# Kernel optimization log

Hardware: AMD Instinct MI355X
Metric: run time of the kernel (lower is better)

## Reference

```python
import jax, jax.numpy as jnp
import numpy as np

NUM_HEADS = 8

def setup_inputs() -> dict:
    key = jax.random.key(0)
    ks = jax.random.split(key, 10)
    B, S, D = 4, 2048, 512
    scale = 1.0 / np.sqrt(D)
    return {
        "x": jax.random.normal(ks[0], (B, S, D), dtype=jnp.float32),
        "q": jax.random.normal(ks[1], (B, S, D), dtype=jnp.float32),
        "Wq": jax.random.normal(ks[2], (D, D), dtype=jnp.float32) * scale,
        "bq": jax.random.normal(ks[3], (D,), dtype=jnp.float32) * 0.01,
        "Wk": jax.random.normal(ks[4], (D, D), dtype=jnp.float32) * scale,
        "bk": jax.random.normal(ks[5], (D,), dtype=jnp.float32) * 0.01,
        "Wv": jax.random.normal(ks[6], (D, D), dtype=jnp.float32) * scale,
        "bv": jax.random.normal(ks[7], (D,), dtype=jnp.float32) * 0.01,
        "Wo": jax.random.normal(ks[8], (D, D), dtype=jnp.float32) * scale,
        "bo": jax.random.normal(ks[9], (D,), dtype=jnp.float32) * 0.01,
    }

def reference(x, q, Wq, bq, Wk, bk, Wv, bv, Wo, bo):
    B, S, D = x.shape
    H = NUM_HEADS
    Dh = D // H
    # Linear layers: y = x @ W.T + b (torch nn.Linear convention)
    def split_heads(t):  # [B,S,D] -> [B,H,S,Dh]
        return t.reshape(B, -1, H, Dh).transpose(0, 2, 1, 3)
    Q = split_heads(q @ Wq.T + bq)
    K = split_heads(x @ Wk.T + bk)
    V = split_heads(x @ Wv.T + bv)
    logits = jnp.einsum('bhqd,bhkd->bhqk', Q, K) / jnp.sqrt(jnp.asarray(Dh, Q.dtype))
    attn = jax.nn.softmax(logits, axis=-1)
    out = jnp.einsum('bhqk,bhkd->bhqd', attn, V)  # [B,H,S,Dh]
    concat = out.transpose(0, 2, 1, 3).reshape(B, -1, D)
    return concat @ Wo.T + bo
```

## Files before the change

kernel.cpp:

```cpp
#include <hip/hip_runtime.h>
#include <stdint.h>

typedef __bf16 bf16_t;
typedef bf16_t bf16x8 __attribute__((ext_vector_type(8)));
typedef bf16_t bf16x4 __attribute__((ext_vector_type(4)));
typedef bf16_t bf16x2 __attribute__((ext_vector_type(2)));
typedef float f32x4 __attribute__((ext_vector_type(4)));
typedef float f32x16 __attribute__((ext_vector_type(16)));
typedef uint32_t u32x4 __attribute__((ext_vector_type(4)));

#define DEV __device__ __forceinline__

DEV void gload_lds16(const void* g, void* l) {
  __builtin_amdgcn_global_load_lds(
      (__attribute__((address_space(1))) void*)(g),
      (__attribute__((address_space(3))) void*)(l), 16, 0, 0);
}

__global__ __launch_bounds__(256) void cvt2_kernel(
    const float* __restrict__ x, const float* __restrict__ q,
    bf16_t* __restrict__ xb, bf16_t* __restrict__ qb) {
  const float* s = blockIdx.y ? q : x;
  bf16_t* d = blockIdx.y ? qb : xb;
  int i = blockIdx.x * 256 + threadIdx.x;
  if (i < 524288) {
    const float4* sp = (const float4*)s + (size_t)i * 2;
    float4 a = sp[0], b = sp[1];
    bf16x8 o;
    o[0] = (bf16_t)a.x; o[1] = (bf16_t)a.y; o[2] = (bf16_t)a.z; o[3] = (bf16_t)a.w;
    o[4] = (bf16_t)b.x; o[5] = (bf16_t)b.y; o[6] = (bf16_t)b.z; o[7] = (bf16_t)b.w;
    *(bf16x8*)(d + (size_t)i * 8) = o;
  }
}

__global__ __launch_bounds__(256) void cvtw_kernel(
    const float* __restrict__ Wq, const float* __restrict__ Wk,
    const float* __restrict__ Wv, const float* __restrict__ Wo,
    bf16_t* __restrict__ dst) {
  int y = blockIdx.y;
  const float* s = (y == 0) ? Wq : (y == 1) ? Wk : (y == 2) ? Wv : Wo;
  bf16_t* d = dst + (size_t)y * 262144;
  int i = blockIdx.x * 256 + threadIdx.x;
  if (i < 32768) {
    const float4* sp = (const float4*)s + (size_t)i * 2;
    float4 a = sp[0], b = sp[1];
    bf16x8 o;
    o[0] = (bf16_t)a.x; o[1] = (bf16_t)a.y; o[2] = (bf16_t)a.z; o[3] = (bf16_t)a.w;
    o[4] = (bf16_t)b.x; o[5] = (bf16_t)b.y; o[6] = (bf16_t)b.z; o[7] = (bf16_t)b.w;
    *(bf16x8*)(d + (size_t)i * 8) = o;
  }
}

DEV void gemm_core(const bf16_t* __restrict__ A, const bf16_t* __restrict__ W,
                   char* smem, f32x4 (&acc)[4][4]) {
  const int tid = threadIdx.x;
  const int lane = tid & 63;
  const int wid = tid >> 6;
  const int wr = wid >> 1, wc = wid & 1;
  const int bx = blockIdx.x, by = blockIdx.y;

  uint32_t goffA[4], goffB[4], ldsoff[4];
#pragma unroll
  for (int c = 0; c < 4; ++c) {
    uint32_t o = (uint32_t)wid * 4096u + (uint32_t)c * 1024u + (uint32_t)lane * 16u;
    uint32_t row = o >> 7;
    uint32_t inner = (o & 127u) ^ ((row & 7u) << 4);
    goffA[c] = ((uint32_t)by * 128u + row) * 1024u + inner;
    goffB[c] = ((uint32_t)bx * 128u + row) * 1024u + inner;
    ldsoff[c] = o - (uint32_t)lane * 16u;
  }
  uint32_t offA[4][2], offB[4][2];
#pragma unroll
  for (int i = 0; i < 4; ++i)
#pragma unroll
    for (int kk = 0; kk < 2; ++kk) {
      uint32_t ra = (uint32_t)(wr * 64 + i * 16 + (lane & 15));
      offA[i][kk] = ra * 128u + (((uint32_t)kk * 64u + ((lane >> 4) * 16u)) ^ ((ra & 7u) << 4));
      uint32_t rb = (uint32_t)(wc * 64 + i * 16 + (lane & 15));
      offB[i][kk] = rb * 128u + (((uint32_t)kk * 64u + ((lane >> 4) * 16u)) ^ ((rb & 7u) << 4));
    }

  const char* Ab = (const char*)A;
  const char* Wb = (const char*)W;

#pragma unroll
  for (int c = 0; c < 4; ++c) {
    gload_lds16(Ab + goffA[c], smem + ldsoff[c]);
    gload_lds16(Wb + goffB[c], smem + 16384 + ldsoff[c]);
  }
  asm volatile("s_waitcnt vmcnt(0)" ::: "memory");
  __syncthreads();

#pragma unroll 1
  for (int kt = 0; kt < 8; ++kt) {
    const int buf = kt & 1;
    char* cur = smem + buf * 32768;
    if (kt < 7) {
      char* nxt = smem + (buf ^ 1) * 32768;
      uint32_t gk = (uint32_t)(kt + 1) * 128u;
#pragma unroll
      for (int c = 0; c < 4; ++c) {
        gload_lds16(Ab + goffA[c] + gk, nxt + ldsoff[c]);
        gload_lds16(Wb + goffB[c] + gk, nxt + 16384 + ldsoff[c]);
      }
    }
    bf16x8 af[4][2], bfr[4][2];
#pragma unroll
    for (int kk = 0; kk < 2; ++kk)
#pragma unroll
      for (int i = 0; i < 4; ++i) {
        af[i][kk] = *(const bf16x8*)(cur + offA[i][kk]);
        bfr[i][kk] = *(const bf16x8*)(cur + 16384 + offB[i][kk]);
      }
    __builtin_amdgcn_s_setprio(1);
#pragma unroll
    for (int kk = 0; kk < 2; ++kk)
#pragma unroll
      for (int mi = 0; mi < 4; ++mi)
#pragma unroll
        for (int nj = 0; nj < 4; ++nj)
          acc[mi][nj] = __builtin_amdgcn_mfma_f32_16x16x32_bf16(
              af[mi][kk], bfr[nj][kk], acc[mi][nj], 0, 0, 0);
    __builtin_amdgcn_s_setprio(0);
    asm volatile("s_waitcnt vmcnt(0)" ::: "memory");
    __syncthreads();
  }
}

__global__ __launch_bounds__(256) void gemm_qkv_kernel(
    const bf16_t* __restrict__ xb, const bf16_t* __restrict__ qb,
    const bf16_t* __restrict__ Wb, const float* __restrict__ bq,
    const float* __restrict__ bk, const float* __restrict__ bv,
    bf16_t* __restrict__ Qh, bf16_t* __restrict__ Kh, bf16_t* __restrict__ VT) {
  __shared__ char smem[65536];
  const int z = blockIdx.z;
  const bf16_t* A = (z == 0) ? qb : xb;
  const bf16_t* W = Wb + (size_t)z * 262144;
  const float* bias = (z == 0) ? bq : (z == 1) ? bk : bv;

  f32x4 acc[4][4] = {};
  gemm_core(A, W, smem, acc);

  const int lane = threadIdx.x & 63, wid = threadIdx.x >> 6;
  const int wr = wid >> 1, wc = wid & 1;
  const int colbase = blockIdx.x * 128 + wc * 64 + (lane & 15);
  const int rowbase = blockIdx.y * 128 + wr * 64 + ((lane >> 4) << 2);

  if (z == 2) {
#pragma unroll
    for (int nj = 0; nj < 4; ++nj) {
      int c = colbase + nj * 16;
      float bb = bias[c];
      int h = c >> 6, d = c & 63;
#pragma unroll
      for (int mi = 0; mi < 4; ++mi) {
        int r0 = rowbase + mi * 16;
        int b = r0 >> 11, s0 = r0 & 2047;
        bf16x4 v;
#pragma unroll
        for (int rr = 0; rr < 4; ++rr) v[rr] = (bf16_t)(acc[mi][nj][rr] + bb);
        *(bf16x4*)(VT + ((size_t)((b << 3) | h) * 64 + d) * 2048 + s0) = v;
      }
    }
  } else {
    bf16_t* O = (z == 0) ? Qh : Kh;
    const float scl = (z == 0) ? 0.18033688f : 1.0f;
#pragma unroll
    for (int nj = 0; nj < 4; ++nj) {
      int c = colbase + nj * 16;
      float bb = bias[c];
      int h = c >> 6, d = c & 63;
#pragma unroll
      for (int mi = 0; mi < 4; ++mi)
#pragma unroll
        for (int rr = 0; rr < 4; ++rr) {
          int r = rowbase + mi * 16 + rr;
          int b = r >> 11, s = r & 2047;
          O[((size_t)((b << 3) | h) * 2048 + s) * 64 + d] = (bf16_t)((acc[mi][nj][rr] + bb) * scl);
        }
    }
  }
}

__global__ __launch_bounds__(256) void gemm_out_kernel(
    const bf16_t* __restrict__ ctx, const bf16_t* __restrict__ Wo,
    const float* __restrict__ bo, float* __restrict__ out) {
  __shared__ char smem[65536];
  f32x4 acc[4][4] = {};
  gemm_core(ctx, Wo, smem, acc);

  const int lane = threadIdx.x & 63, wid = threadIdx.x >> 6;
  const int wr = wid >> 1, wc = wid & 1;
  const int colbase = blockIdx.x * 128 + wc * 64 + (lane & 15);
  const int rowbase = blockIdx.y * 128 + wr * 64 + ((lane >> 4) << 2);
#pragma unroll
  for (int nj = 0; nj < 4; ++nj) {
    int c = colbase + nj * 16;
    float bb = bo[c];
#pragma unroll
    for (int mi = 0; mi < 4; ++mi)
#pragma unroll
      for (int rr = 0; rr < 4; ++rr) {
        int r = rowbase + mi * 16 + rr;
        out[(size_t)r * 512 + c] = acc[mi][nj][rr] + bb;
      }
  }
}

__global__ __launch_bounds__(256, 2) void attn_kernel(
    const bf16_t* __restrict__ Qh, const bf16_t* __restrict__ Kh,
    const bf16_t* __restrict__ VT, bf16_t* __restrict__ ctx) {
  __shared__ char smem[32768];
  char* Kb = smem;
  char* Vb = smem + 16384;
  const int tid = threadIdx.x, lane = tid & 63, wid = tid >> 6;
  const int l31 = lane & 31, h = lane >> 5;
  const int qt = blockIdx.x, bh = blockIdx.y;

  const char* Kbase = (const char*)Kh + (size_t)bh * 262144;
  const char* Vbase = (const char*)VT + (size_t)bh * 262144;
  const char* Qbase = (const char*)Qh + (size_t)bh * 262144;

  const int qrow = qt * 128 + wid * 32 + l31;
  bf16x8 qf[4];
#pragma unroll
  for (int ks = 0; ks < 4; ++ks)
    qf[ks] = *(const bf16x8*)(Qbase + (size_t)qrow * 128 + ks * 32 + h * 16);

  uint32_t kgo[2], vgo[2], lo[2];
#pragma unroll
  for (int c = 0; c < 2; ++c) {
    uint32_t o = (uint32_t)c * 4096u + (uint32_t)wid * 1024u + (uint32_t)lane * 16u;
    uint32_t row = o >> 7;
    uint32_t inner = (o & 127u) ^ ((row & 7u) << 4);
    kgo[c] = row * 128u + inner;
    vgo[c] = row * 4096u + inner;
    lo[c] = o - (uint32_t)lane * 16u;
  }

  const uint32_t swz = (uint32_t)(l31 & 7) << 4;
  uint32_t fbase[2], fcol[4];
#pragma unroll
  for (int c = 0; c < 2; ++c) fbase[c] = (uint32_t)(32 * c + l31) * 128u;
#pragma unroll
  for (int ks = 0; ks < 4; ++ks) fcol[ks] = ((uint32_t)(ks * 32 + h * 16)) ^ swz;

  f32x16 oacc[2] = {};
  float m_run = -1.0e30f, l_part = 0.f;

#pragma unroll
  for (int c = 0; c < 2; ++c) {
    gload_lds16(Kbase + kgo[c], Kb + lo[c]);
    gload_lds16(Vbase + vgo[c], Vb + lo[c]);
  }
  asm volatile("s_waitcnt vmcnt(0)" ::: "memory");
  __syncthreads();

#pragma unroll 1
  for (int t = 0; t < 32; ++t) {
    const uint32_t cur = ((uint32_t)t & 1u) << 13;
    if (t < 31) {
      const uint32_t nxt = cur ^ 8192u;
      const char* Kn = Kbase + (size_t)(t + 1) * 8192;
      const char* Vn = Vbase + (size_t)(t + 1) * 128;
#pragma unroll
      for (int c = 0; c < 2; ++c) {
        gload_lds16(Kn + kgo[c], Kb + nxt + lo[c]);
        gload_lds16(Vn + vgo[c], Vb + nxt + lo[c]);
      }
    }

    f32x16 sT[2] = {};
#pragma unroll
    for (int c = 0; c < 2; ++c) {
      __builtin_amdgcn_s_setprio(1);
#pragma unroll
      for (int ks = 0; ks < 4; ++ks) {
        bf16x8 kf = *(const bf16x8*)(Kb + cur + fbase[c] + fcol[ks]);
        sT[c] = __builtin_amdgcn_mfma_f32_32x32x16_bf16(kf, qf[ks], sT[c], 0, 0, 0);
      }
      __builtin_amdgcn_s_setprio(0);
    }

    float mx = sT[0][0];
#pragma unroll
    for (int c = 0; c < 2; ++c)
#pragma unroll
      for (int r = 0; r < 16; ++r) mx = fmaxf(mx, sT[c][r]);
    mx = fmaxf(mx, __shfl_xor(mx, 32));
    bool ok = (mx <= m_run + 8.0f);
    if (!__all(ok)) {
      float mnew = fmaxf(m_run, mx);
      float sc = __builtin_exp2f(m_run - mnew);
      m_run = mnew;
      l_part *= sc;
#pragma unroll
      for (int r = 0; r < 16; ++r) { oacc[0][r] *= sc; oacc[1][r] *= sc; }
    }

    uint32_t cw[2][8];
    float ladd = 0.f;
#pragma unroll
    for (int c = 0; c < 2; ++c)
#pragma unroll
      for (int w = 0; w < 8; ++w) {
        float p0 = __builtin_exp2f(sT[c][2 * w] - m_run);
        float p1 = __builtin_exp2f(sT[c][2 * w + 1] - m_run);
        ladd += p0 + p1;
        bf16x2 tp; tp[0] = (bf16_t)p0; tp[1] = (bf16_t)p1;
        cw[c][w] = __builtin_bit_cast(uint32_t, tp);
      }
    l_part += ladd;

    bf16x8 pa[4];
#pragma unroll
    for (int s = 0; s < 4; ++s) {
      const int c = s >> 1, sp = s & 1;
      uint32_t w0 = cw[c][4 * sp + 0], w1 = cw[c][4 * sp + 1];
      uint32_t w2 = cw[c][4 * sp + 2], w3 = cw[c][4 * sp + 3];
      uint32_t sx0 = (uint32_t)__shfl_xor((int)w0, 32);
      uint32_t sx1 = (uint32_t)__shfl_xor((int)w1, 32);
      uint32_t sx2 = (uint32_t)__shfl_xor((int)w2, 32);
      uint32_t sx3 = (uint32_t)__shfl_xor((int)w3, 32);
      u32x4 ta;
      ta[0] = h ? sx2 : w0;
      ta[1] = h ? sx3 : w1;
      ta[2] = h ? w2 : sx0;
      ta[3] = h ? w3 : sx1;
      pa[s] = __builtin_bit_cast(bf16x8, ta);
    }

#pragma unroll
    for (int dc = 0; dc < 2; ++dc) {
      __builtin_amdgcn_s_setprio(1);
#pragma unroll
      for (int ks = 0; ks < 4; ++ks) {
        bf16x8 vf = *(const bf16x8*)(Vb + cur + fbase[dc] + fcol[ks]);
        oacc[dc] = __builtin_amdgcn_mfma_f32_32x32x16_bf16(vf, pa[ks], oacc[dc], 0, 0, 0);
      }
      __builtin_amdgcn_s_setprio(0);
    }

    asm volatile("s_waitcnt vmcnt(0)" ::: "memory");
    __syncthreads();
  }

  float l = l_part + __shfl_xor(l_part, 32);
  float inv = 1.0f / l;
  const int b = bh >> 3, hh = bh & 7;
  bf16_t* crow = ctx + ((size_t)(b * 2048 + qrow)) * 512 + hh * 64;
#pragma unroll
  for (int dc = 0; dc < 2; ++dc)
#pragma unroll
    for (int m = 0; m < 4; ++m) {
      bf16x4 v;
#pragma unroll
      for (int r = 0; r < 4; ++r) v[r] = (bf16_t)(oacc[dc][4 * m + r] * inv);
      *(bf16x4*)(crow + dc * 32 + m * 8 + h * 4) = v;
    }
}

extern "C" void kernel_launch(void* const* d_in, const int* in_sizes, int n_in,
                              void* d_out, int out_size, void* d_ws, size_t ws_size,
                              hipStream_t stream) {
  const float* x  = (const float*)d_in[0];
  const float* q  = (const float*)d_in[1];
  const float* Wq = (const float*)d_in[2];
  const float* bq = (const float*)d_in[3];
  const float* Wk = (const float*)d_in[4];
  const float* bk = (const float*)d_in[5];
  const float* Wv = (const float*)d_in[6];
  const float* bv = (const float*)d_in[7];
  const float* Wo = (const float*)d_in[8];
  const float* bo = (const float*)d_in[9];

  char* ws = (char*)d_ws;
  bf16_t* xb  = (bf16_t*)(ws + 0);
  bf16_t* qb  = (bf16_t*)(ws + 8388608);
  bf16_t* Wb  = (bf16_t*)(ws + 16777216);
  bf16_t* Qh  = (bf16_t*)(ws + 18874368);
  bf16_t* Kh  = (bf16_t*)(ws + 27262976);
  bf16_t* VT  = (bf16_t*)(ws + 35651584);
  bf16_t* ctx = (bf16_t*)(ws + 44040192);

  cvt2_kernel<<<dim3(2048, 2), 256, 0, stream>>>(x, q, xb, qb);
  cvtw_kernel<<<dim3(128, 4), 256, 0, stream>>>(Wq, Wk, Wv, Wo, Wb);
  gemm_qkv_kernel<<<dim3(4, 64, 3), 256, 0, stream>>>(xb, qb, Wb, bq, bk, bv, Qh, Kh, VT);
  attn_kernel<<<dim3(16, 32), 256, 0, stream>>>(Qh, Kh, VT, ctx);
  gemm_out_kernel<<<dim3(4, 64), 256, 0, stream>>>(ctx, Wb + 3 * 262144, bo, (float*)d_out);
}
```

Baseline: 121.2 us.

## Quad-buffer K/V tiles with prefetch distance two and lazy max rescaling

The attention kernel moves from double to four-stage LDS buffering of K/V tiles (64KB shared), prefetching two tiles ahead and waiting with partial vmcnt counts. This replaces the per-iteration full drain and syncthreads with a single barrier at the top of each iteration. It also drops the per-tile row-max reduction: exponentials are computed against the running max, and the max and rescale pass only run when a partial sum passes a threshold. The larger LDS footprint may limit blocks per CU, and the recompute path adds cost whenever it triggers.

Measured after the change: 124.6 us. +2.8%, slower.

```diff
diff --git a/kernel.cpp b/kernel.cpp
--- a/kernel.cpp
+++ b/kernel.cpp
@@ -210,9 +210,7 @@
 __global__ __launch_bounds__(256, 2) void attn_kernel(
     const bf16_t* __restrict__ Qh, const bf16_t* __restrict__ Kh,
     const bf16_t* __restrict__ VT, bf16_t* __restrict__ ctx) {
-  __shared__ char smem[32768];
-  char* Kb = smem;
-  char* Vb = smem + 16384;
+  __shared__ char smem[65536];
   const int tid = threadIdx.x, lane = tid & 63, wid = tid >> 6;
   const int l31 = lane & 31, h = lane >> 5;
   const int qt = blockIdx.x, bh = blockIdx.y;
@@ -249,26 +247,36 @@
   float m_run = -1.0e30f, l_part = 0.f;
 
 #pragma unroll
-  for (int c = 0; c < 2; ++c) {
-    gload_lds16(Kbase + kgo[c], Kb + lo[c]);
-    gload_lds16(Vbase + vgo[c], Vb + lo[c]);
-  }
-  asm volatile("s_waitcnt vmcnt(0)" ::: "memory");
-  __syncthreads();
+  for (int tt = 0; tt < 2; ++tt) {
+    const uint32_t b = (uint32_t)tt * 16384u;
+    const char* Kt = Kbase + (size_t)tt * 8192;
+    const char* Vt = Vbase + (size_t)tt * 128;
+#pragma unroll
+    for (int c = 0; c < 2; ++c) {
+      gload_lds16(Kt + kgo[c], smem + b + lo[c]);
+      gload_lds16(Vt + vgo[c], smem + b + 8192 + lo[c]);
+    }
+  }
 
 #pragma unroll 1
   for (int t = 0; t < 32; ++t) {
-    const uint32_t cur = ((uint32_t)t & 1u) << 13;
-    if (t < 31) {
-      const uint32_t nxt = cur ^ 8192u;
-      const char* Kn = Kbase + (size_t)(t + 1) * 8192;
-      const char* Vn = Vbase + (size_t)(t + 1) * 128;
+    const uint32_t cur = ((uint32_t)t & 3u) * 16384u;
+    if (t < 30) {
+      const uint32_t nb = ((uint32_t)(t + 2) & 3u) * 16384u;
+      const char* Kn = Kbase + (size_t)(t + 2) * 8192;
+      const char* Vn = Vbase + (size_t)(t + 2) * 128;
 #pragma unroll
       for (int c = 0; c < 2; ++c) {
-        gload_lds16(Kn + kgo[c], Kb + nxt + lo[c]);
-        gload_lds16(Vn + vgo[c], Vb + nxt + lo[c]);
-      }
-    }
+        gload_lds16(Kn + kgo[c], smem + nb + lo[c]);
+        gload_lds16(Vn + vgo[c], smem + nb + 8192 + lo[c]);
+      }
+      asm volatile("s_waitcnt vmcnt(8)" ::: "memory");
+    } else if (t == 30) {
+      asm volatile("s_waitcnt vmcnt(4)" ::: "memory");
+    } else {
+      asm volatile("s_waitcnt vmcnt(0)" ::: "memory");
+    }
+    __builtin_amdgcn_s_barrier();
 
     f32x16 sT[2] = {};
 #pragma unroll
@@ -276,26 +284,10 @@
       __builtin_amdgcn_s_setprio(1);
 #pragma unroll
       for (int ks = 0; ks < 4; ++ks) {
-        bf16x8 kf = *(const bf16x8*)(Kb + cur + fbase[c] + fcol[ks]);
+        bf16x8 kf = *(const bf16x8*)(smem + cur + fbase[c] + fcol[ks]);
         sT[c] = __builtin_amdgcn_mfma_f32_32x32x16_bf16(kf, qf[ks], sT[c], 0, 0, 0);
       }
       __builtin_amdgcn_s_setprio(0);
-    }
-
-    float mx = sT[0][0];
-#pragma unroll
-    for (int c = 0; c < 2; ++c)
-#pragma unroll
-      for (int r = 0; r < 16; ++r) mx = fmaxf(mx, sT[c][r]);
-    mx = fmaxf(mx, __shfl_xor(mx, 32));
-    bool ok = (mx <= m_run + 8.0f);
-    if (!__all(ok)) {
-      float mnew = fmaxf(m_run, mx);
-      float sc = __builtin_exp2f(m_run - mnew);
-      m_run = mnew;
-      l_part *= sc;
-#pragma unroll
-      for (int r = 0; r < 16; ++r) { oacc[0][r] *= sc; oacc[1][r] *= sc; }
     }
 
     uint32_t cw[2][8];
@@ -310,6 +302,31 @@
         bf16x2 tp; tp[0] = (bf16_t)p0; tp[1] = (bf16_t)p1;
         cw[c][w] = __builtin_bit_cast(uint32_t, tp);
       }
+    if (!__all(ladd <= 16384.0f)) {
+      float mx = sT[0][0];
+#pragma unroll
+      for (int c = 0; c < 2; ++c)
+#pragma unroll
+        for (int r = 0; r < 16; ++r) mx = fmaxf(mx, sT[c][r]);
+      mx = fmaxf(mx, __shfl_xor(mx, 32));
+      float mnew = fmaxf(m_run, mx);
+      float sc = __builtin_exp2f(m_run - mnew);
+      l_part *= sc;
+#pragma unroll
+      for (int r = 0; r < 16; ++r) { oacc[0][r] *= sc; oacc[1][r] *= sc; }
+      m_run = mnew;
+      ladd = 0.f;
+#pragma unroll
+      for (int c = 0; c < 2; ++c)
+#pragma unroll
+        for (int w = 0; w < 8; ++w) {
+          float p0 = __builtin_exp2f(sT[c][2 * w] - m_run);
+          float p1 = __builtin_exp2f(sT[c][2 * w + 1] - m_run);
+          ladd += p0 + p1;
+          bf16x2 tp; tp[0] = (bf16_t)p0; tp[1] = (bf16_t)p1;
+          cw[c][w] = __builtin_bit_cast(uint32_t, tp);
+        }
+    }
     l_part += ladd;
 
     bf16x8 pa[4];
@@ -335,14 +352,11 @@
       __builtin_amdgcn_s_setprio(1);
 #pragma unroll
       for (int ks = 0; ks < 4; ++ks) {
-        bf16x8 vf = *(const bf16x8*)(Vb + cur + fbase[dc] + fcol[ks]);
+        bf16x8 vf = *(const bf16x8*)(smem + cur + 8192 + fbase[dc] + fcol[ks]);
         oacc[dc] = __builtin_amdgcn_mfma_f32_32x32x16_bf16(vf, pa[ks], oacc[dc], 0, 0, 0);
       }
       __builtin_amdgcn_s_setprio(0);
     }
-
-    asm volatile("s_waitcnt vmcnt(0)" ::: "memory");
-    __syncthreads();
   }
 
   float l = l_part + __shfl_xor(l_part, 32);
```

## Split attention KV sequence in two with a combine kernel and lazy rescaling

Applied to the files above, without the earlier changes.

Splits the key/value sequence across two blocks per query tile (split-K flash attention), so each block writes unnormalized partial outputs plus running max and sum, and a new combine kernel merges them into ctx. The goal is to double the attention grid to fill the GPU better, and the occupancy hint is raised to 4 blocks per SM. The online softmax now skips computing the max unless the exp sum exceeds a threshold, in which case it rescales and recomputes. The cost is an extra kernel launch, extra global traffic for the partial outputs, and bf16 rounding of the unnormalized partials.

After: 297.6 us. 146% more time.

```diff
diff --git a/kernel.cpp b/kernel.cpp
--- a/kernel.cpp
+++ b/kernel.cpp
@@ -207,18 +207,19 @@
   }
 }
 
-__global__ __launch_bounds__(256, 2) void attn_kernel(
+__global__ __launch_bounds__(256, 4) void attn_kernel(
     const bf16_t* __restrict__ Qh, const bf16_t* __restrict__ Kh,
-    const bf16_t* __restrict__ VT, bf16_t* __restrict__ ctx) {
+    const bf16_t* __restrict__ VT, bf16_t* __restrict__ Opart,
+    float2* __restrict__ ml) {
   __shared__ char smem[32768];
   char* Kb = smem;
   char* Vb = smem + 16384;
   const int tid = threadIdx.x, lane = tid & 63, wid = tid >> 6;
   const int l31 = lane & 31, h = lane >> 5;
-  const int qt = blockIdx.x, bh = blockIdx.y;
-
-  const char* Kbase = (const char*)Kh + (size_t)bh * 262144;
-  const char* Vbase = (const char*)VT + (size_t)bh * 262144;
+  const int qt = blockIdx.x, bh = blockIdx.y, sp = blockIdx.z;
+
+  const char* Kbase = (const char*)Kh + (size_t)bh * 262144 + (size_t)sp * 131072;
+  const char* Vbase = (const char*)VT + (size_t)bh * 262144 + (size_t)sp * 2048;
   const char* Qbase = (const char*)Qh + (size_t)bh * 262144;
 
   const int qrow = qt * 128 + wid * 32 + l31;
@@ -257,9 +258,9 @@
   __syncthreads();
 
 #pragma unroll 1
-  for (int t = 0; t < 32; ++t) {
+  for (int t = 0; t < 16; ++t) {
     const uint32_t cur = ((uint32_t)t & 1u) << 13;
-    if (t < 31) {
+    if (t < 15) {
       const uint32_t nxt = cur ^ 8192u;
       const char* Kn = Kbase + (size_t)(t + 1) * 8192;
       const char* Vn = Vbase + (size_t)(t + 1) * 128;
@@ -282,42 +283,59 @@
       __builtin_amdgcn_s_setprio(0);
     }
 
-    float mx = sT[0][0];
-#pragma unroll
-    for (int c = 0; c < 2; ++c)
-#pragma unroll
-      for (int r = 0; r < 16; ++r) mx = fmaxf(mx, sT[c][r]);
-    mx = fmaxf(mx, __shfl_xor(mx, 32));
-    bool ok = (mx <= m_run + 8.0f);
-    if (!__all(ok)) {
-      float mnew = fmaxf(m_run, mx);
-      float sc = __builtin_exp2f(m_run - mnew);
-      m_run = mnew;
-      l_part *= sc;
-#pragma unroll
-      for (int r = 0; r < 16; ++r) { oacc[0][r] *= sc; oacc[1][r] *= sc; }
-    }
-
     uint32_t cw[2][8];
-    float ladd = 0.f;
+    float la0 = 0.f, la1 = 0.f, la2 = 0.f, la3 = 0.f;
 #pragma unroll
     for (int c = 0; c < 2; ++c)
 #pragma unroll
       for (int w = 0; w < 8; ++w) {
         float p0 = __builtin_exp2f(sT[c][2 * w] - m_run);
         float p1 = __builtin_exp2f(sT[c][2 * w + 1] - m_run);
-        ladd += p0 + p1;
+        if ((w & 3) == 0) la0 += p0 + p1;
+        else if ((w & 3) == 1) la1 += p0 + p1;
+        else if ((w & 3) == 2) la2 += p0 + p1;
+        else la3 += p0 + p1;
         bf16x2 tp; tp[0] = (bf16_t)p0; tp[1] = (bf16_t)p1;
         cw[c][w] = __builtin_bit_cast(uint32_t, tp);
       }
+    float ladd = (la0 + la1) + (la2 + la3);
+    if (!__all(ladd <= 16384.0f)) {
+      float mx = sT[0][0];
+#pragma unroll
+      for (int c = 0; c < 2; ++c)
+#pragma unroll
+        for (int r = 0; r < 16; ++r) mx = fmaxf(mx, sT[c][r]);
+      mx = fmaxf(mx, __shfl_xor(mx, 32));
+      float mnew = fmaxf(m_run, mx);
+      float sc = __builtin_exp2f(m_run - mnew);
+      l_part *= sc;
+#pragma unroll
+      for (int r = 0; r < 16; ++r) { oacc[0][r] *= sc; oacc[1][r] *= sc; }
+      m_run = mnew;
+      la0 = la1 = la2 = la3 = 0.f;
+#pragma unroll
+      for (int c = 0; c < 2; ++c)
+#pragma unroll
+        for (int w = 0; w < 8; ++w) {
+          float p0 = __builtin_exp2f(sT[c][2 * w] - m_run);
+          float p1 = __builtin_exp2f(sT[c][2 * w + 1] - m_run);
+          if ((w & 3) == 0) la0 += p0 + p1;
+          else if ((w & 3) == 1) la1 += p0 + p1;
+          else if ((w & 3) == 2) la2 += p0 + p1;
+          else la3 += p0 + p1;
+          bf16x2 tp; tp[0] = (bf16_t)p0; tp[1] = (bf16_t)p1;
+          cw[c][w] = __builtin_bit_cast(uint32_t, tp);
+        }
+      ladd = (la0 + la1) + (la2 + la3);
+    }
     l_part += ladd;
 
     bf16x8 pa[4];
 #pragma unroll
     for (int s = 0; s < 4; ++s) {
-      const int c = s >> 1, sp = s & 1;
-      uint32_t w0 = cw[c][4 * sp + 0], w1 = cw[c][4 * sp + 1];
-      uint32_t w2 = cw[c][4 * sp + 2], w3 = cw[c][4 * sp + 3];
+      const int c = s >> 1, spp = s & 1;
+      uint32_t w0 = cw[c][4 * spp + 0], w1 = cw[c][4 * spp + 1];
+      uint32_t w2 = cw[c][4 * spp + 2], w3 = cw[c][4 * spp + 3];
       uint32_t sx0 = (uint32_t)__shfl_xor((int)w0, 32);
       uint32_t sx1 = (uint32_t)__shfl_xor((int)w1, 32);
       uint32_t sx2 = (uint32_t)__shfl_xor((int)w2, 32);
@@ -346,18 +364,39 @@
   }
 
   float l = l_part + __shfl_xor(l_part, 32);
-  float inv = 1.0f / l;
-  const int b = bh >> 3, hh = bh & 7;
-  bf16_t* crow = ctx + ((size_t)(b * 2048 + qrow)) * 512 + hh * 64;
+  const size_t prow = (size_t)sp * 65536 + (size_t)bh * 2048 + qrow;
+  if (h == 0) ml[prow] = make_float2(m_run, l);
+  bf16_t* orow = Opart + prow * 64;
 #pragma unroll
   for (int dc = 0; dc < 2; ++dc)
 #pragma unroll
     for (int m = 0; m < 4; ++m) {
       bf16x4 v;
 #pragma unroll
-      for (int r = 0; r < 4; ++r) v[r] = (bf16_t)(oacc[dc][4 * m + r] * inv);
-      *(bf16x4*)(crow + dc * 32 + m * 8 + h * 4) = v;
-    }
+      for (int r = 0; r < 4; ++r) v[r] = (bf16_t)(oacc[dc][4 * m + r]);
+      *(bf16x4*)(orow + dc * 32 + m * 8 + h * 4) = v;
+    }
+}
+
+__global__ __launch_bounds__(256) void combine_kernel(
+    const bf16_t* __restrict__ Opart, const float2* __restrict__ ml,
+    bf16_t* __restrict__ ctx) {
+  int g = blockIdx.x * 256 + threadIdx.x;
+  int row = g >> 3, d0 = (g & 7) * 8;
+  float2 ml0 = ml[row], ml1 = ml[row + 65536];
+  float mmax = fmaxf(ml0.x, ml1.x);
+  float a0 = __builtin_exp2f(ml0.x - mmax);
+  float a1 = __builtin_exp2f(ml1.x - mmax);
+  float inv = 1.0f / (a0 * ml0.y + a1 * ml1.y);
+  float s0 = a0 * inv, s1 = a1 * inv;
+  bf16x8 o0 = *(const bf16x8*)(Opart + (size_t)row * 64 + d0);
+  bf16x8 o1 = *(const bf16x8*)(Opart + (size_t)(row + 65536) * 64 + d0);
+  bf16x8 o;
+#pragma unroll
+  for (int i = 0; i < 8; ++i) o[i] = (bf16_t)((float)o0[i] * s0 + (float)o1[i] * s1);
+  int bh = row >> 11, qr = row & 2047;
+  int b = bh >> 3, hh = bh & 7;
+  *(bf16x8*)(ctx + ((size_t)(b * 2048 + qr)) * 512 + hh * 64 + d0) = o;
 }
 
 extern "C" void kernel_launch(void* const* d_in, const int* in_sizes, int n_in,
@@ -375,17 +414,20 @@
   const float* bo = (const float*)d_in[9];
 
   char* ws = (char*)d_ws;
-  bf16_t* xb  = (bf16_t*)(ws + 0);
-  bf16_t* qb  = (bf16_t*)(ws + 8388608);
-  bf16_t* Wb  = (bf16_t*)(ws + 16777216);
-  bf16_t* Qh  = (bf16_t*)(ws + 18874368);
-  bf16_t* Kh  = (bf16_t*)(ws + 27262976);
-  bf16_t* VT  = (bf16_t*)(ws + 35651584);
-  bf16_t* ctx = (bf16_t*)(ws + 44040192);
+  bf16_t* xb    = (bf16_t*)(ws + 0);
+  bf16_t* qb    = (bf16_t*)(ws + 8388608);
+  bf16_t* Wb    = (bf16_t*)(ws + 16777216);
+  bf16_t* Qh    = (bf16_t*)(ws + 18874368);
+  bf16_t* Kh    = (bf16_t*)(ws + 27262976);
+  bf16_t* VT    = (bf16_t*)(ws + 35651584);
+  bf16_t* ctx   = (bf16_t*)(ws + 44040192);
+  bf16_t* Opart = (bf16_t*)(ws + 52428800);
+  float2* mlb   = (float2*)(ws + 69206016);
 
   cvt2_kernel<<<dim3(2048, 2), 256, 0, stream>>>(x, q, xb, qb);
   cvtw_kernel<<<dim3(128, 4), 256, 0, stream>>>(Wq, Wk, Wv, Wo, Wb);
   gemm_qkv_kernel<<<dim3(4, 64, 3), 256, 0, stream>>>(xb, qb, Wb, bq, bk, bv, Qh, Kh, VT);
-  attn_kernel<<<dim3(16, 32), 256, 0, stream>>>(Qh, Kh, VT, ctx);
+  attn_kernel<<<dim3(16, 32, 2), 256, 0, stream>>>(Qh, Kh, VT, Opart, mlb);
+  combine_kernel<<<2048, 256, 0, stream>>>(Opart, mlb, ctx);
   gemm_out_kernel<<<dim3(4, 64), 256, 0, stream>>>(ctx, Wb + 3 * 262144, bo, (float*)d_out);
 }
```

## Double KV tile to 128 keys and defer max computation in attention

Applied to the files above, without the earlier changes.

The attention kernel now processes 128 keys per iteration instead of 64, doubling LDS to 64KB, halving loop iterations and barriers, and changing the V-tile swizzle to 256-byte rows. The online softmax no longer computes the row max up front. It exponentiates against the running max and only computes the max, rescales and recomputes when a partial sum exceeds a threshold. This removes per-tile max reductions and synchronisation but raises register and LDS pressure, which may hurt occupancy at 2 blocks per CU, and adds a costly recompute path when the max grows.

Result: slower. 139.0 us (+14.6%).

```diff
diff --git a/kernel.cpp b/kernel.cpp
--- a/kernel.cpp
+++ b/kernel.cpp
@@ -210,9 +210,7 @@
 __global__ __launch_bounds__(256, 2) void attn_kernel(
     const bf16_t* __restrict__ Qh, const bf16_t* __restrict__ Kh,
     const bf16_t* __restrict__ VT, bf16_t* __restrict__ ctx) {
-  __shared__ char smem[32768];
-  char* Kb = smem;
-  char* Vb = smem + 16384;
+  __shared__ char smem[65536];
   const int tid = threadIdx.x, lane = tid & 63, wid = tid >> 6;
   const int l31 = lane & 31, h = lane >> 5;
   const int qt = blockIdx.x, bh = blockIdx.y;
@@ -227,94 +225,114 @@
   for (int ks = 0; ks < 4; ++ks)
     qf[ks] = *(const bf16x8*)(Qbase + (size_t)qrow * 128 + ks * 32 + h * 16);
 
-  uint32_t kgo[2], vgo[2], lo[2];
-#pragma unroll
-  for (int c = 0; c < 2; ++c) {
+  uint32_t kgo[4], vgo[4], lo[4];
+#pragma unroll
+  for (int c = 0; c < 4; ++c) {
     uint32_t o = (uint32_t)c * 4096u + (uint32_t)wid * 1024u + (uint32_t)lane * 16u;
-    uint32_t row = o >> 7;
-    uint32_t inner = (o & 127u) ^ ((row & 7u) << 4);
-    kgo[c] = row * 128u + inner;
-    vgo[c] = row * 4096u + inner;
+    uint32_t krow = o >> 7;
+    kgo[c] = krow * 128u + ((o & 127u) ^ ((krow & 7u) << 4));
+    uint32_t vrow = o >> 8;
+    vgo[c] = vrow * 4096u + ((o & 255u) ^ ((vrow & 15u) << 4));
     lo[c] = o - (uint32_t)lane * 16u;
   }
 
-  const uint32_t swz = (uint32_t)(l31 & 7) << 4;
-  uint32_t fbase[2], fcol[4];
-#pragma unroll
-  for (int c = 0; c < 2; ++c) fbase[c] = (uint32_t)(32 * c + l31) * 128u;
-#pragma unroll
-  for (int ks = 0; ks < 4; ++ks) fcol[ks] = ((uint32_t)(ks * 32 + h * 16)) ^ swz;
+  const uint32_t swzK = (uint32_t)(l31 & 7) << 4;
+  uint32_t kcol[4];
+#pragma unroll
+  for (int ks = 0; ks < 4; ++ks) kcol[ks] = ((uint32_t)(ks * 32 + h * 16)) ^ swzK;
+  const uint32_t swzV = (uint32_t)(l31 & 15) << 4;
+  uint32_t vcol[8];
+#pragma unroll
+  for (int s = 0; s < 8; ++s) vcol[s] = ((uint32_t)(s * 32 + h * 16)) ^ swzV;
 
   f32x16 oacc[2] = {};
   float m_run = -1.0e30f, l_part = 0.f;
 
 #pragma unroll
-  for (int c = 0; c < 2; ++c) {
-    gload_lds16(Kbase + kgo[c], Kb + lo[c]);
-    gload_lds16(Vbase + vgo[c], Vb + lo[c]);
+  for (int c = 0; c < 4; ++c) {
+    gload_lds16(Kbase + kgo[c], smem + lo[c]);
+    gload_lds16(Vbase + vgo[c], smem + 32768 + lo[c]);
   }
   asm volatile("s_waitcnt vmcnt(0)" ::: "memory");
   __syncthreads();
 
 #pragma unroll 1
-  for (int t = 0; t < 32; ++t) {
-    const uint32_t cur = ((uint32_t)t & 1u) << 13;
-    if (t < 31) {
-      const uint32_t nxt = cur ^ 8192u;
-      const char* Kn = Kbase + (size_t)(t + 1) * 8192;
-      const char* Vn = Vbase + (size_t)(t + 1) * 128;
-#pragma unroll
-      for (int c = 0; c < 2; ++c) {
-        gload_lds16(Kn + kgo[c], Kb + nxt + lo[c]);
-        gload_lds16(Vn + vgo[c], Vb + nxt + lo[c]);
-      }
-    }
-
-    f32x16 sT[2] = {};
-#pragma unroll
-    for (int c = 0; c < 2; ++c) {
-      __builtin_amdgcn_s_setprio(1);
+  for (int t = 0; t < 16; ++t) {
+    const uint32_t cur = ((uint32_t)t & 1u) * 16384u;
+    char* Kc = smem + cur;
+    char* Vc = smem + 32768 + cur;
+    if (t < 15) {
+      const uint32_t nxt = cur ^ 16384u;
+      const char* Kn = Kbase + (size_t)(t + 1) * 16384;
+      const char* Vn = Vbase + (size_t)(t + 1) * 256;
+#pragma unroll
+      for (int c = 0; c < 4; ++c) {
+        gload_lds16(Kn + kgo[c], smem + nxt + lo[c]);
+        gload_lds16(Vn + vgo[c], smem + 32768 + nxt + lo[c]);
+      }
+    }
+
+    f32x16 sT[4] = {};
+    __builtin_amdgcn_s_setprio(1);
+#pragma unroll
+    for (int c = 0; c < 4; ++c)
 #pragma unroll
       for (int ks = 0; ks < 4; ++ks) {
-        bf16x8 kf = *(const bf16x8*)(Kb + cur + fbase[c] + fcol[ks]);
+        bf16x8 kf = *(const bf16x8*)(Kc + (uint32_t)(32 * c + l31) * 128u + kcol[ks]);
         sT[c] = __builtin_amdgcn_mfma_f32_32x32x16_bf16(kf, qf[ks], sT[c], 0, 0, 0);
       }
-      __builtin_amdgcn_s_setprio(0);
-    }
-
-    float mx = sT[0][0];
-#pragma unroll
-    for (int c = 0; c < 2; ++c)
-#pragma unroll
-      for (int r = 0; r < 16; ++r) mx = fmaxf(mx, sT[c][r]);
-    mx = fmaxf(mx, __shfl_xor(mx, 32));
-    bool ok = (mx <= m_run + 8.0f);
-    if (!__all(ok)) {
-      float mnew = fmaxf(m_run, mx);
-      float sc = __builtin_exp2f(m_run - mnew);
-      m_run = mnew;
-      l_part *= sc;
-#pragma unroll
-      for (int r = 0; r < 16; ++r) { oacc[0][r] *= sc; oacc[1][r] *= sc; }
-    }
-
-    uint32_t cw[2][8];
-    float ladd = 0.f;
-#pragma unroll
-    for (int c = 0; c < 2; ++c)
+    __builtin_amdgcn_s_setprio(0);
+
+    uint32_t cw[4][8];
+    float la0 = 0.f, la1 = 0.f, la2 = 0.f, la3 = 0.f;
+#pragma unroll
+    for (int c = 0; c < 4; ++c)
 #pragma unroll
       for (int w = 0; w < 8; ++w) {
         float p0 = __builtin_exp2f(sT[c][2 * w] - m_run);
         float p1 = __builtin_exp2f(sT[c][2 * w + 1] - m_run);
-        ladd += p0 + p1;
+        if ((w & 3) == 0) la0 += p0 + p1;
+        else if ((w & 3) == 1) la1 += p0 + p1;
+        else if ((w & 3) == 2) la2 += p0 + p1;
+        else la3 += p0 + p1;
         bf16x2 tp; tp[0] = (bf16_t)p0; tp[1] = (bf16_t)p1;
         cw[c][w] = __builtin_bit_cast(uint32_t, tp);
       }
+    float ladd = (la0 + la1) + (la2 + la3);
+    if (!__all(ladd <= 16384.0f)) {
+      float mx = sT[0][0];
+#pragma unroll
+      for (int c = 0; c < 4; ++c)
+#pragma unroll
+        for (int r = 0; r < 16; ++r) mx = fmaxf(mx, sT[c][r]);
+      mx = fmaxf(mx, __shfl_xor(mx, 32));
+      float mnew = fmaxf(m_run, mx);
+      float sc = __builtin_exp2f(m_run - mnew);
+      l_part *= sc;
+#pragma unroll
+      for (int r = 0; r < 16; ++r) { oacc[0][r] *= sc; oacc[1][r] *= sc; }
+      m_run = mnew;
+      la0 = la1 = la2 = la3 = 0.f;
+#pragma unroll
+      for (int c = 0; c < 4; ++c)
+#pragma unroll
+        for (int w = 0; w < 8; ++w) {
+          float p0 = __builtin_exp2f(sT[c][2 * w] - m_run);
+          float p1 = __builtin_exp2f(sT[c][2 * w + 1] - m_run);
+          if ((w & 3) == 0) la0 += p0 + p1;
+          else if ((w & 3) == 1) la1 += p0 + p1;
+          else if ((w & 3) == 2) la2 += p0 + p1;
+          else la3 += p0 + p1;
+          bf16x2 tp; tp[0] = (bf16_t)p0; tp[1] = (bf16_t)p1;
+          cw[c][w] = __builtin_bit_cast(uint32_t, tp);
+        }
+      ladd = (la0 + la1) + (la2 + la3);
+    }
     l_part += ladd;
 
-    bf16x8 pa[4];
-#pragma unroll
-    for (int s = 0; s < 4; ++s) {
+    bf16x8 pa[8];
+#pragma unroll
+    for (int s = 0; s < 8; ++s) {
       const int c = s >> 1, sp = s & 1;
       uint32_t w0 = cw[c][4 * sp + 0], w1 = cw[c][4 * sp + 1];
       uint32_t w2 = cw[c][4 * sp + 2], w3 = cw[c][4 * sp + 3];
@@ -330,16 +348,15 @@
       pa[s] = __builtin_bit_cast(bf16x8, ta);
     }
 
-#pragma unroll
-    for (int dc = 0; dc < 2; ++dc) {
-      __builtin_amdgcn_s_setprio(1);
-#pragma unroll
-      for (int ks = 0; ks < 4; ++ks) {
-        bf16x8 vf = *(const bf16x8*)(Vb + cur + fbase[dc] + fcol[ks]);
-        oacc[dc] = __builtin_amdgcn_mfma_f32_32x32x16_bf16(vf, pa[ks], oacc[dc], 0, 0, 0);
-      }
-      __builtin_amdgcn_s_setprio(0);
-    }
+    __builtin_amdgcn_s_setprio(1);
+#pragma unroll
+    for (int dc = 0; dc < 2; ++dc)
+#pragma unroll
+      for (int s = 0; s < 8; ++s) {
+        bf16x8 vf = *(const bf16x8*)(Vc + (uint32_t)(32 * dc + l31) * 256u + vcol[s]);
+        oacc[dc] = __builtin_amdgcn_mfma_f32_32x32x16_bf16(vf, pa[s], oacc[dc], 0, 0, 0);
+      }
+    __builtin_amdgcn_s_setprio(0);
 
     asm volatile("s_waitcnt vmcnt(0)" ::: "memory");
     __syncthreads();
```
